# Optimization experiments

Hardware: AMD Instinct MI355X
Metric: run time of the kernel (lower is better)

The kernel has to match this reference:

```python
import jax, jax.numpy as jnp
import numpy as np

B, T, D, H, DFF = 2, 2048, 1024, 16, 4096
K = D // H  # head size = 64
EPS = 1e-5


def _layernorm(x, g, b):
    mu = jnp.mean(x, axis=-1, keepdims=True)
    var = jnp.mean(jnp.square(x - mu), axis=-1, keepdims=True)
    return (x - mu) * jax.lax.rsqrt(var + EPS) * g + b


def setup_inputs() -> dict:
    key = jax.random.key(0)
    ks = jax.random.split(key, 12)
    s_attn = 1.0 / np.sqrt(D)
    s_ff1 = 1.0 / np.sqrt(D)
    s_ff2 = 1.0 / np.sqrt(DFF)
    return {
        "x": jax.random.normal(ks[0], (B, T, D), jnp.float32),
        # per-head q/k/v projections, stacked: [H, D, K] (each head's Linear has no bias)
        "Wq": jax.random.normal(ks[1], (H, D, K), jnp.float32) * s_attn,
        "Wk": jax.random.normal(ks[2], (H, D, K), jnp.float32) * s_attn,
        "Wv": jax.random.normal(ks[3], (H, D, K), jnp.float32) * s_attn,
        "Wo": jax.random.normal(ks[4], (D, D), jnp.float32) * s_attn,
        "bo": jax.random.normal(ks[5], (D,), jnp.float32) * 0.01,
        "W1": jax.random.normal(ks[6], (D, DFF), jnp.float32) * s_ff1,
        "b1": jax.random.normal(ks[7], (DFF,), jnp.float32) * 0.01,
        "W2": jax.random.normal(ks[8], (DFF, D), jnp.float32) * s_ff2,
        "b2": jax.random.normal(ks[9], (D,), jnp.float32) * 0.01,
        "g1": jnp.ones((D,), jnp.float32),
        "be1": jnp.zeros((D,), jnp.float32),
        "g2": jnp.ones((D,), jnp.float32),
        "be2": jnp.zeros((D,), jnp.float32),
    }


def reference(x, Wq, Wk, Wv, Wo, bo, W1, b1, W2, b2, g1, be1, g2, be2):
    b, t, d = x.shape
    h = _layernorm(x, g1, be1)
    # multi-head attention (per-head linear projections, fused via einsum)
    q = jnp.einsum('btd,hdk->bhtk', h, Wq)
    k = jnp.einsum('btd,hdk->bhtk', h, Wk)
    v = jnp.einsum('btd,hdk->bhtk', h, Wv)
    scores = jnp.einsum('bhtk,bhsk->bhts', q, k) * (K ** -0.5)
    causal = jnp.tril(jnp.ones((t, t), bool))
    scores = jnp.where(causal, scores, -jnp.inf)
    attn = jax.nn.softmax(scores, axis=-1)
    o = jnp.einsum('bhts,bhsk->bhtk', attn, v)
    o = o.transpose(0, 2, 1, 3).reshape(b, t, d)  # concat heads
    x = x + o @ Wo + bo
    # feed-forward (exact GELU, as torch default)
    h2 = _layernorm(x, g2, be2)
    ff = jax.nn.gelu(h2 @ W1 + b1, approximate=False) @ W2 + b2
    return x + ff
```

## Files before the change

kernel.cpp:

```cpp
#include <hip/hip_runtime.h>
#include <hip/hip_bf16.h>


#define BT   4096
#define DIM  1024
#define DFF  4096
#define TSEQ 2048
#define NHEAD 16
#define HDIM 64
#define QKV_LD 3072

typedef __attribute__((ext_vector_type(8))) short  bf16x8;
typedef __attribute__((ext_vector_type(4))) float  floatx4;

__device__ __forceinline__ void async_copy16(const __hip_bfloat16* g, __hip_bfloat16* l) {
    __builtin_amdgcn_global_load_lds(
        (const __attribute__((address_space(1))) void*)g,
        (__attribute__((address_space(3))) void*)l, 16, 0, 0);
}

__device__ __forceinline__ floatx4 mfma_bf16(bf16x8 a, bf16x8 b, floatx4 c) {
    return __builtin_amdgcn_mfma_f32_16x16x32_bf16(a, b, c, 0, 0, 0);
}

__global__ __launch_bounds__(256) void ln_kernel(const float* __restrict__ x,
                                                 const float* __restrict__ g,
                                                 const float* __restrict__ be,
                                                 __hip_bfloat16* __restrict__ out) {
    const int row = blockIdx.x;
    const int t = threadIdx.x;
    const float4 v = ((const float4*)(x + (size_t)row * DIM))[t];
    float s  = v.x + v.y + v.z + v.w;
    float ss = v.x * v.x + v.y * v.y + v.z * v.z + v.w * v.w;
    for (int d = 1; d < 64; d <<= 1) { s += __shfl_xor(s, d); ss += __shfl_xor(ss, d); }
    __shared__ float red[8];
    const int w = t >> 6;
    if ((t & 63) == 0) { red[w] = s; red[w + 4] = ss; }
    __syncthreads();
    s  = red[0] + red[1] + red[2] + red[3];
    ss = red[4] + red[5] + red[6] + red[7];
    const float mu = s * (1.0f / DIM);
    const float rstd = rsqrtf(ss * (1.0f / DIM) - mu * mu + 1e-5f);
    const float4 gv = ((const float4*)g)[t];
    const float4 bv = ((const float4*)be)[t];
    __hip_bfloat16* o = out + (size_t)row * DIM + t * 4;
    o[0] = __float2bfloat16((v.x - mu) * rstd * gv.x + bv.x);
    o[1] = __float2bfloat16((v.y - mu) * rstd * gv.y + bv.y);
    o[2] = __float2bfloat16((v.z - mu) * rstd * gv.z + bv.z);
    o[3] = __float2bfloat16((v.w - mu) * rstd * gv.w + bv.w);
}

__global__ __launch_bounds__(256) void transpose_cast(const float* __restrict__ src, int src_ld,
                                                      __hip_bfloat16* __restrict__ dst, int dst_ld) {
    __shared__ float tile[64][65];
    const int r0 = blockIdx.x * 64, c0 = blockIdx.y * 64;
    const int tr = threadIdx.x >> 6;
    const int tc = threadIdx.x & 63;
    for (int i = 0; i < 16; ++i) {
        const int r = i * 4 + tr;
        tile[r][tc] = src[(size_t)(r0 + r) * src_ld + c0 + tc];
    }
    __syncthreads();
    for (int i = 0; i < 16; ++i) {
        const int c = i * 4 + tr;
        dst[(size_t)(c0 + c) * dst_ld + r0 + tc] = __float2bfloat16(tile[tc][c]);
    }
}

__global__ __launch_bounds__(256) void transpose_qkv(const float* __restrict__ Wq,
                                                     const float* __restrict__ Wk,
                                                     const float* __restrict__ Wv,
                                                     __hip_bfloat16* __restrict__ dst) {
    __shared__ float tile[64][65];
    const int hz = blockIdx.y;
    const int proj = hz >> 4, h = hz & 15;
    const float* W = (proj == 0 ? Wq : (proj == 1 ? Wk : Wv)) + (size_t)h * DIM * HDIM;
    const int r0 = blockIdx.x * 64;
    const int tr = threadIdx.x >> 6;
    const int tc = threadIdx.x & 63;
    for (int i = 0; i < 16; ++i) {
        const int r = i * 4 + tr;
        tile[r][tc] = W[(size_t)(r0 + r) * HDIM + tc];
    }
    __syncthreads();
    for (int i = 0; i < 16; ++i) {
        const int k = i * 4 + tr;
        dst[(size_t)(proj * 1024 + h * 64 + k) * DIM + r0 + tc] = __float2bfloat16(tile[tc][k]);
    }
}

__global__ __launch_bounds__(256) void transpose_v(const __hip_bfloat16* __restrict__ qkv,
                                                   __hip_bfloat16* __restrict__ vt) {
    __shared__ __align__(16) __hip_bfloat16 tile[64 * 72];
    const int t = threadIdx.x;
    const int bh = blockIdx.y;
    const int b = bh >> 4, h = bh & 15;
    const int t0 = blockIdx.x * 64;
    const __hip_bfloat16* src = qkv + (size_t)b * TSEQ * QKV_LD + 2048 + h * HDIM;
    const int lo = t >> 3, k8 = t & 7;
    for (int i = 0; i < 2; ++i) {
        const int rr = i * 32 + lo;
        const bf16x8 v = *(const bf16x8*)(src + (size_t)(t0 + rr) * QKV_LD + k8 * 8);
        const int cb = k8 ^ ((rr >> 3) & 7);
        *(bf16x8*)(tile + rr * 72 + cb * 8) = v;
    }
    __syncthreads();
    for (int i = 0; i < 2; ++i) {
        const int dd = i * 32 + lo;
        const int c0 = dd >> 3, cl = dd & 7;
        bf16x8 o;
        for (int jj = 0; jj < 8; ++jj) {
            const int key = k8 * 8 + jj;
            o[jj] = *(const short*)(tile + key * 72 + (c0 ^ ((key >> 3) & 7)) * 8 + cl);
        }
        *(bf16x8*)(vt + ((size_t)bh * HDIM + dd) * TSEQ + t0 + k8 * 8) = o;
    }
}

template <int EPI>
__global__ __launch_bounds__(256) void gemm_bt(const __hip_bfloat16* __restrict__ A,
                                               const __hip_bfloat16* __restrict__ Bt,
                                               __hip_bfloat16* __restrict__ outb,
                                               const float* __restrict__ bias,
                                               int M, int N, int K) {
    __shared__ __align__(16) __hip_bfloat16 As[128 * 32];
    __shared__ __align__(16) __hip_bfloat16 Bs[128 * 32];
    const int t = threadIdx.x;
    const int w = t >> 6, l = t & 63;
    const int quad = l >> 4, tl = l & 15;
    const int wr = w >> 1, wc = w & 1;
    const int m0 = blockIdx.y * 128, n0 = blockIdx.x * 128;

    floatx4 acc[4][4] = {};
    const int rowA = t >> 2;
    const int c8 = (t & 3) << 3;

    for (int k0 = 0; k0 < K; k0 += 32) {
        __syncthreads();
        {
            const __hip_bfloat16* gA = A + (size_t)(m0 + rowA) * K + k0 + c8;
            const __hip_bfloat16* gB = Bt + (size_t)(n0 + rowA) * K + k0 + c8;
            async_copy16(gA,                  As + w * 512);
            async_copy16(gA + (size_t)64 * K, As + 2048 + w * 512);
            async_copy16(gB,                  Bs + w * 512);
            async_copy16(gB + (size_t)64 * K, Bs + 2048 + w * 512);
        }
        __syncthreads();

        bf16x8 af[4], bfr[4];
        const int aRow = wr * 64 + tl;
        const int bRow = wc * 64 + tl;
        for (int mi = 0; mi < 4; ++mi)
            af[mi] = *(const bf16x8*)(As + (aRow + mi * 16) * 32 + quad * 8);
        for (int ni = 0; ni < 4; ++ni)
            bfr[ni] = *(const bf16x8*)(Bs + (bRow + ni * 16) * 32 + quad * 8);
        for (int mi = 0; mi < 4; ++mi)
            for (int ni = 0; ni < 4; ++ni)
                acc[mi][ni] = mfma_bf16(af[mi], bfr[ni], acc[mi][ni]);
    }

    const int rowBase = m0 + wr * 64 + quad * 4;
    const int colBase = n0 + wc * 64 + tl;
    for (int mi = 0; mi < 4; ++mi) {
        for (int ni = 0; ni < 4; ++ni) {
            const int c = colBase + ni * 16;
            for (int j = 0; j < 4; ++j) {
                const int r = rowBase + mi * 16 + j;
                const size_t idx = (size_t)r * N + c;
                float v = acc[mi][ni][j];
                if (EPI == 1) {
                    v += bias[c];
                    v = 0.5f * v * (1.0f + erff(v * 0.70710678118654752f));
                }
                outb[idx] = __float2bfloat16(v);
            }
        }
    }
}

__global__ __launch_bounds__(256) void gemm_bt_k64(const __hip_bfloat16* __restrict__ A,
                                                   const __hip_bfloat16* __restrict__ Bt,
                                                   float* __restrict__ outf,
                                                   const float* __restrict__ bias,
                                                   const float* __restrict__ resid,
                                                   int M, int N, int K) {
    __shared__ __align__(16) __hip_bfloat16 As[128 * 64];
    __shared__ __align__(16) __hip_bfloat16 Bs[64 * 64];
    const int t = threadIdx.x;
    const int w = t >> 6, l = t & 63;
    const int quad = l >> 4, tl = l & 15;
    const int id = blockIdx.x;
    const int xcd = id & 7, jb = id >> 3;
    const int n0 = (jb & 15) * 64;
    const int m0 = ((jb >> 4) * 8 + xcd) * 128;

    floatx4 acc[2][4] = {};
    const int srow = t >> 3;
    const int scg  = t & 7;

    for (int k0 = 0; k0 < K; k0 += 64) {
        __syncthreads();
        for (int i = 0; i < 4; ++i) {
            const int row = i * 32 + srow;
            async_copy16(A + (size_t)(m0 + row) * K + k0 + ((scg ^ (row & 7)) << 3),
                         As + i * 2048 + w * 512);
        }
        for (int i = 0; i < 2; ++i) {
            const int row = i * 32 + srow;
            async_copy16(Bt + (size_t)(n0 + row) * K + k0 + ((scg ^ (row & 7)) << 3),
                         Bs + i * 2048 + w * 512);
        }
        __syncthreads();

        for (int ks = 0; ks < 2; ++ks) {
            bf16x8 af[2], bfr[4];
            for (int mi = 0; mi < 2; ++mi) {
                const int r = w * 32 + mi * 16 + tl;
                af[mi] = *(const bf16x8*)(As + r * 64 + (((ks * 4 + quad) ^ (r & 7)) << 3));
            }
            for (int ni = 0; ni < 4; ++ni) {
                const int r = ni * 16 + tl;
                bfr[ni] = *(const bf16x8*)(Bs + r * 64 + (((ks * 4 + quad) ^ (r & 7)) << 3));
            }
            for (int mi = 0; mi < 2; ++mi)
                for (int ni = 0; ni < 4; ++ni)
                    acc[mi][ni] = mfma_bf16(af[mi], bfr[ni], acc[mi][ni]);
        }
    }

    const int rowBase = m0 + w * 32 + quad * 4;
    const int colBase = n0 + tl;
    for (int mi = 0; mi < 2; ++mi) {
        for (int ni = 0; ni < 4; ++ni) {
            const int c = colBase + ni * 16;
            for (int j = 0; j < 4; ++j) {
                const int r = rowBase + mi * 16 + j;
                const size_t idx = (size_t)r * N + c;
                outf[idx] = resid[idx] + acc[mi][ni][j] + bias[c];
            }
        }
    }
}

#define KS_LD 72
#define VT_LD 72
#define PL_LD 72
__global__ __launch_bounds__(256) void attn_kernel(const __hip_bfloat16* __restrict__ qkv,
                                                   const __hip_bfloat16* __restrict__ vt,
                                                   __hip_bfloat16* __restrict__ out) {
    __shared__ __align__(16) __hip_bfloat16 Ks[64 * KS_LD];
    __shared__ __align__(16) __hip_bfloat16 Vts[64 * VT_LD];
    __shared__ __align__(16) __hip_bfloat16 Pl[4][16 * PL_LD];
    const int t = threadIdx.x;
    const int w = t >> 6, l = t & 63;
    const int quad = l >> 4, tl = l & 15;
    const int id = blockIdx.x;
    const int bh = ((id & 7) << 2) | ((id >> 3) & 3);
    const int pq = id >> 5;
    const int b = bh >> 4, h = bh & 15;
    const __hip_bfloat16* Qp  = qkv + (size_t)b * TSEQ * QKV_LD + h * HDIM;
    const __hip_bfloat16* Kp  = Qp + 1024;
    const __hip_bfloat16* Vtp = vt + (size_t)bh * HDIM * TSEQ;
    __hip_bfloat16* P = Pl[w];
    const float cscale = 0.125f * 1.4426950408889634f;
    const int srow = t >> 3, sk8 = t & 7;

    for (int half = 0; half < 2; ++half) {
        const int qb = half ? (31 - pq) : pq;
        const int qw = qb * 64 + w * 16;
        const int nb = qb + 1;

        const __hip_bfloat16* qrow = Qp + (size_t)(qw + tl) * QKV_LD + quad * 8;
        const bf16x8 qf0 = *(const bf16x8*)qrow;
        const bf16x8 qf1 = *(const bf16x8*)(qrow + 32);
        floatx4 oacc[4] = {};
        float l_i[4] = {0.0f, 0.0f, 0.0f, 0.0f};
        const int myrow = quad * 4;

        for (int it = 0; it < nb; ++it) {
            const int s0 = it * 64;
            __syncthreads();
            for (int i = 0; i < 2; ++i) {
                const int rr = i * 32 + srow;
                const bf16x8 kv = *(const bf16x8*)(Kp  + (size_t)(s0 + rr) * QKV_LD + sk8 * 8);
                const bf16x8 vv = *(const bf16x8*)(Vtp + (size_t)rr * TSEQ + s0 + sk8 * 8);
                *(bf16x8*)(Ks  + rr * KS_LD + sk8 * 8) = kv;
                *(bf16x8*)(Vts + rr * VT_LD + sk8 * 8) = vv;
            }
            __syncthreads();

            floatx4 sc[4];
            for (int ni = 0; ni < 4; ++ni) {
                const __hip_bfloat16* kr = Ks + (ni * 16 + tl) * KS_LD + quad * 8;
                floatx4 z = {0.0f, 0.0f, 0.0f, 0.0f};
                z = mfma_bf16(qf0, *(const bf16x8*)kr, z);
                sc[ni] = mfma_bf16(qf1, *(const bf16x8*)(kr + 32), z);
            }

            const bool lastB = (it == nb - 1);
            for (int ni = 0; ni < 4; ++ni) {
                const int keyrel = ni * 16 + tl - w * 16;
                for (int j = 0; j < 4; ++j) {
                    float pv = exp2f(sc[ni][j] * cscale);
                    if (lastB && keyrel > myrow + j) pv = 0.0f;
                    l_i[j] += pv;
                    P[(myrow + j) * PL_LD + ni * 16 + tl] = __float2bfloat16(pv);
                }
            }
            __builtin_amdgcn_wave_barrier();

            for (int kc = 0; kc < 2; ++kc) {
                const bf16x8 pf = *(const bf16x8*)(P + tl * PL_LD + kc * 32 + quad * 8);
                for (int ni = 0; ni < 4; ++ni) {
                    const bf16x8 vf = *(const bf16x8*)(Vts + (ni * 16 + tl) * VT_LD
                                                       + kc * 32 + quad * 8);
                    oacc[ni] = mfma_bf16(pf, vf, oacc[ni]);
                }
            }
        }

        for (int d = 1; d < 16; d <<= 1) {
            float r0 = __shfl_xor(l_i[0], d), r1 = __shfl_xor(l_i[1], d);
            float r2 = __shfl_xor(l_i[2], d), r3 = __shfl_xor(l_i[3], d);
            l_i[0] += r0; l_i[1] += r1; l_i[2] += r2; l_i[3] += r3;
        }
        for (int j = 0; j < 4; ++j) {
            const float inv = 1.0f / l_i[j];
            const int rg = qw + quad * 4 + j;
            __hip_bfloat16* orow = out + ((size_t)b * TSEQ + rg) * DIM + h * HDIM;
            for (int ni = 0; ni < 4; ++ni)
                orow[ni * 16 + tl] = __float2bfloat16(oacc[ni][j] * inv);
        }
    }
}

extern "C" void kernel_launch(void* const* d_in, const int* in_sizes, int n_in,
                              void* d_out, int out_size, void* d_ws, size_t ws_size,
                              hipStream_t stream) {
    const float* x   = (const float*)d_in[0];
    const float* Wq  = (const float*)d_in[1];
    const float* Wk  = (const float*)d_in[2];
    const float* Wv  = (const float*)d_in[3];
    const float* Wo  = (const float*)d_in[4];
    const float* bo  = (const float*)d_in[5];
    const float* W1  = (const float*)d_in[6];
    const float* b1  = (const float*)d_in[7];
    const float* W2  = (const float*)d_in[8];
    const float* b2  = (const float*)d_in[9];
    const float* g1  = (const float*)d_in[10];
    const float* be1 = (const float*)d_in[11];
    const float* g2  = (const float*)d_in[12];
    const float* be2 = (const float*)d_in[13];
    float* out = (float*)d_out;

    size_t off = 0;
    char* wsb = (char*)d_ws;
    auto carve = [&](size_t bytes) {
        void* p = wsb + off;
        off += (bytes + 255) & ~(size_t)255;
        return p;
    };
    __hip_bfloat16* WqkvT = (__hip_bfloat16*)carve((size_t)3072 * 1024 * 2);
    __hip_bfloat16* WoT   = (__hip_bfloat16*)carve((size_t)1024 * 1024 * 2);
    __hip_bfloat16* W1T   = (__hip_bfloat16*)carve((size_t)4096 * 1024 * 2);
    __hip_bfloat16* W2T   = (__hip_bfloat16*)carve((size_t)1024 * 4096 * 2);
    __hip_bfloat16* h1    = (__hip_bfloat16*)carve((size_t)BT * DIM * 2);
    __hip_bfloat16* qkv   = (__hip_bfloat16*)carve((size_t)BT * QKV_LD * 2);
    __hip_bfloat16* vtb   = (__hip_bfloat16*)carve((size_t)BT * DIM * 2);
    __hip_bfloat16* att   = (__hip_bfloat16*)carve((size_t)BT * DIM * 2);
    float*          x2    = (float*)carve((size_t)BT * DIM * 4);
    __hip_bfloat16* h2    = (__hip_bfloat16*)carve((size_t)BT * DIM * 2);
    __hip_bfloat16* ff1   = (__hip_bfloat16*)carve((size_t)BT * DFF * 2);

    transpose_qkv<<<dim3(16, 48), 256, 0, stream>>>(Wq, Wk, Wv, WqkvT);
    transpose_cast<<<dim3(16, 16), 256, 0, stream>>>(Wo, 1024, WoT, 1024);
    transpose_cast<<<dim3(16, 64), 256, 0, stream>>>(W1, 4096, W1T, 1024);
    transpose_cast<<<dim3(64, 16), 256, 0, stream>>>(W2, 1024, W2T, 4096);

    ln_kernel<<<BT, 256, 0, stream>>>(x, g1, be1, h1);
    gemm_bt<0><<<dim3(24, 32), 256, 0, stream>>>(h1, WqkvT, qkv, nullptr, BT, QKV_LD, DIM);
    transpose_v<<<dim3(32, 32), 256, 0, stream>>>(qkv, vtb);
    attn_kernel<<<512, 256, 0, stream>>>(qkv, vtb, att);
    gemm_bt_k64<<<512, 256, 0, stream>>>(att, WoT, x2, bo, x, BT, DIM, DIM);
    ln_kernel<<<BT, 256, 0, stream>>>(x2, g2, be2, h2);
    gemm_bt<1><<<dim3(32, 32), 256, 0, stream>>>(h2, W1T, ff1, b1, BT, DFF, DIM);
    gemm_bt_k64<<<512, 256, 0, stream>>>(ff1, W2T, out, b2, x2, BT, DIM, DFF);
}
```

Before: 385.4 us.

## Widen GEMM K-tile to 64 with XOR-swizzled LDS and staged epilogue

The bf16 GEMM kernel now loads 64-wide K slices into XOR-swizzled shared memory, so each wave issues two MFMA sub-steps per barrier pair and avoids LDS bank conflicts on fragment reads. This halves the number of synchronisation rounds in the K loop. The epilogue loads the bias once per column, writes the bf16 results into a padded LDS tile, and stores them back in half-tiles as 16-byte row-contiguous chunks instead of scattered 2-byte stores. In exchange it uses twice the shared memory and adds extra barriers in the epilogue. The 132-element row pitch also makes the 16-byte LDS reads unaligned on odd rows, which may be slow.

```diff
diff --git a/kernel.cpp b/kernel.cpp
--- a/kernel.cpp
+++ b/kernel.cpp
@@ -123,8 +123,9 @@
                                                __hip_bfloat16* __restrict__ outb,
                                                const float* __restrict__ bias,
                                                int M, int N, int K) {
-    __shared__ __align__(16) __hip_bfloat16 As[128 * 32];
-    __shared__ __align__(16) __hip_bfloat16 Bs[128 * 32];
+    __shared__ __align__(16) __hip_bfloat16 smem[2 * 128 * 64];
+    __hip_bfloat16* As = smem;
+    __hip_bfloat16* Bs = smem + 128 * 64;
     const int t = threadIdx.x;
     const int w = t >> 6, l = t & 63;
     const int quad = l >> 4, tl = l & 15;
@@ -132,48 +133,63 @@
     const int m0 = blockIdx.y * 128, n0 = blockIdx.x * 128;
 
     floatx4 acc[4][4] = {};
-    const int rowA = t >> 2;
-    const int c8 = (t & 3) << 3;
-
-    for (int k0 = 0; k0 < K; k0 += 32) {
-        __syncthreads();
-        {
-            const __hip_bfloat16* gA = A + (size_t)(m0 + rowA) * K + k0 + c8;
-            const __hip_bfloat16* gB = Bt + (size_t)(n0 + rowA) * K + k0 + c8;
-            async_copy16(gA,                  As + w * 512);
-            async_copy16(gA + (size_t)64 * K, As + 2048 + w * 512);
-            async_copy16(gB,                  Bs + w * 512);
-            async_copy16(gB + (size_t)64 * K, Bs + 2048 + w * 512);
-        }
-        __syncthreads();
-
-        bf16x8 af[4], bfr[4];
-        const int aRow = wr * 64 + tl;
-        const int bRow = wc * 64 + tl;
-        for (int mi = 0; mi < 4; ++mi)
-            af[mi] = *(const bf16x8*)(As + (aRow + mi * 16) * 32 + quad * 8);
+    const int srow = t >> 3;
+    const int scg  = t & 7;
+
+    for (int k0 = 0; k0 < K; k0 += 64) {
+        __syncthreads();
+        for (int i = 0; i < 4; ++i) {
+            const int row = i * 32 + srow;
+            const int off = (scg ^ (row & 7)) << 3;
+            async_copy16(A  + (size_t)(m0 + row) * K + k0 + off, As + i * 2048 + w * 512);
+            async_copy16(Bt + (size_t)(n0 + row) * K + k0 + off, Bs + i * 2048 + w * 512);
+        }
+        __syncthreads();
+
+        for (int ks = 0; ks < 2; ++ks) {
+            bf16x8 af[4], bfr[4];
+            for (int mi = 0; mi < 4; ++mi) {
+                const int r = wr * 64 + mi * 16 + tl;
+                af[mi] = *(const bf16x8*)(As + r * 64 + (((ks * 4 + quad) ^ (r & 7)) << 3));
+            }
+            for (int ni = 0; ni < 4; ++ni) {
+                const int r = wc * 64 + ni * 16 + tl;
+                bfr[ni] = *(const bf16x8*)(Bs + r * 64 + (((ks * 4 + quad) ^ (r & 7)) << 3));
+            }
+            for (int mi = 0; mi < 4; ++mi)
+                for (int ni = 0; ni < 4; ++ni)
+                    acc[mi][ni] = mfma_bf16(af[mi], bfr[ni], acc[mi][ni]);
+        }
+    }
+
+    float bs[4];
+    if (EPI == 1)
         for (int ni = 0; ni < 4; ++ni)
-            bfr[ni] = *(const bf16x8*)(Bs + (bRow + ni * 16) * 32 + quad * 8);
-        for (int mi = 0; mi < 4; ++mi)
-            for (int ni = 0; ni < 4; ++ni)
-                acc[mi][ni] = mfma_bf16(af[mi], bfr[ni], acc[mi][ni]);
-    }
-
-    const int rowBase = m0 + wr * 64 + quad * 4;
-    const int colBase = n0 + wc * 64 + tl;
-    for (int mi = 0; mi < 4; ++mi) {
-        for (int ni = 0; ni < 4; ++ni) {
-            const int c = colBase + ni * 16;
-            for (int j = 0; j < 4; ++j) {
-                const int r = rowBase + mi * 16 + j;
-                const size_t idx = (size_t)r * N + c;
-                float v = acc[mi][ni][j];
-                if (EPI == 1) {
-                    v += bias[c];
-                    v = 0.5f * v * (1.0f + erff(v * 0.70710678118654752f));
+            bs[ni] = bias[n0 + wc * 64 + ni * 16 + tl];
+    __hip_bfloat16* Cs = smem;
+    const int orow = t >> 4, ocl = t & 15;
+    for (int p = 0; p < 2; ++p) {
+        __syncthreads();
+        if (wr == p) {
+            for (int mi = 0; mi < 4; ++mi) {
+                for (int ni = 0; ni < 4; ++ni) {
+                    for (int j = 0; j < 4; ++j) {
+                        float v = acc[mi][ni][j];
+                        if (EPI == 1) {
+                            v += bs[ni];
+                            v = 0.5f * v * (1.0f + erff(v * 0.70710678118654752f));
+                        }
+                        Cs[(mi * 16 + quad * 4 + j) * 132 + wc * 64 + ni * 16 + tl] =
+                            __float2bfloat16(v);
+                    }
                 }
-                outb[idx] = __float2bfloat16(v);
-            }
+            }
+        }
+        __syncthreads();
+        for (int i = 0; i < 4; ++i) {
+            const int rr = i * 16 + orow;
+            const bf16x8 vv = *(const bf16x8*)(Cs + rr * 132 + ocl * 8);
+            *(bf16x8*)(outb + (size_t)(m0 + p * 64 + rr) * N + n0 + ocl * 8) = vv;
         }
     }
 }
```

After: 409.0 us. 1.06x slower.
